# Kernel tuning notes

Hardware: AMD Instinct MI355X
Metric: run time of the kernel (lower is better)

Reference implementation:

```python
import jax, jax.numpy as jnp
import numpy as np

D_MODEL = 1024
N_HEADS = 16
HEAD_DIM = D_MODEL // N_HEADS


def setup_inputs() -> dict:
    key = jax.random.key(0)
    k1, k2, k3 = jax.random.split(key, 3)
    x = jax.random.normal(k1, (2, 2048, D_MODEL), dtype=jnp.float32)
    w_qkv = jax.random.normal(k2, (3 * D_MODEL, D_MODEL), dtype=jnp.float32) * 0.02
    w_out = jax.random.normal(k3, (D_MODEL, D_MODEL), dtype=jnp.float32) * 0.02
    return {"x": x, "w_qkv": w_qkv, "w_out": w_out}


def reference(x, w_qkv, w_out):
    B, T, D = x.shape
    H, Hd = N_HEADS, HEAD_DIM
    # QKV projection: Linear stores weight as [out, in] -> '...i,oi->...o'
    qkv = jnp.einsum('bti,oi->bto', x, w_qkv)              # [B, T, 3D]
    # split (3*H, Hs) group-major, chunk into q/k/v of H heads each
    qkv = qkv.reshape(B, T, 3, H, Hd)
    q = jnp.transpose(qkv[:, :, 0], (0, 2, 1, 3))          # [B, H, T, Hd]
    k = jnp.transpose(qkv[:, :, 1], (0, 2, 1, 3))
    v = jnp.transpose(qkv[:, :, 2], (0, 2, 1, 3))
    scale = 1.0 / jnp.sqrt(jnp.asarray(Hd, dtype=x.dtype))
    scores = jnp.einsum('bhqd,bhkd->bhqk', q, k) * scale   # [B, H, T, T]
    causal = jnp.tril(jnp.ones((T, T), dtype=bool))        # [T, T]
    scores = jnp.where(causal[None, None], scores, jnp.asarray(-jnp.inf, dtype=scores.dtype))
    attn = jax.nn.softmax(scores, axis=-1)
    ctx = jnp.einsum('bhqk,bhkd->bhqd', attn, v)           # [B, H, T, Hd]
    ctx = jnp.transpose(ctx, (0, 2, 1, 3)).reshape(B, T, D)
    return jnp.einsum('bti,oi->bto', ctx, w_out)
```

## Files before the change

kernel.cpp:

```cpp
#include <hip/hip_runtime.h>


typedef short short8 __attribute__((ext_vector_type(8)));
typedef float f32x4 __attribute__((ext_vector_type(4)));
typedef unsigned short u16;
typedef unsigned int u32;

#define T_SEQ 2048
#define N_B 2
#define N_H 16
#define HD 64
#define DM 1024
#define TRIPLE 3072

__device__ __forceinline__ u16 f2bf(float f) {
  union { float f; unsigned u; } v;
  v.f = f;
  unsigned r = v.u + 0x7fffu + ((v.u >> 16) & 1u);
  return (u16)(r >> 16);
}

__device__ __forceinline__ float bf2f(u16 x) {
  return __uint_as_float((u32)x << 16);
}

__device__ __forceinline__ u32 cvtpk(float a, float b) {
  u32 r;
  asm("v_cvt_pk_bf16_f32 %0, %1, %2" : "=v"(r) : "v"(a), "v"(b));
  return r;
}

typedef const __attribute__((address_space(1))) void gvoid;
typedef __attribute__((address_space(3))) void lvoid;

__device__ __forceinline__ void g2l16(const void* g, void* l) {
  __builtin_amdgcn_global_load_lds((gvoid*)g, (lvoid*)l, 16, 0, 0);
}

__device__ __forceinline__ void storeC(float* p, float v) { *p = v; }
__device__ __forceinline__ void storeC(u16* p, float v) { *p = f2bf(v); }

__global__ __launch_bounds__(256) void cast_all(const float4* __restrict__ x,
                                                const float4* __restrict__ wq,
                                                const float4* __restrict__ wo,
                                                ushort4* __restrict__ out) {
  int i = blockIdx.x * 256 + threadIdx.x;
  const float4* src;
  int off;
  if (i < 1048576) { src = x; off = 0; }
  else if (i < 1835008) { src = wq; off = 1048576; }
  else { src = wo; off = 1835008; }
  float4 v = src[i - off];
  ushort4 o;
  o.x = f2bf(v.x); o.y = f2bf(v.y); o.z = f2bf(v.z); o.w = f2bf(v.w);
  out[i] = o;
}

__global__ __launch_bounds__(256) void vtrans(const u16* __restrict__ qkv,
                                              u16* __restrict__ vT) {
  const int tid = threadIdx.x;
  const int w = tid >> 6, lane = tid & 63;
  const int ti = lane >> 3, di = lane & 7;
  const int h = blockIdx.y, b = blockIdx.z;
  const int t0 = blockIdx.x * 256 + w * 64 + ti * 8;

  const u16* src = qkv + (size_t)(b * T_SEQ + t0) * TRIPLE + 2 * DM + h * HD + di * 8;
  u32 x[8][4];
#pragma unroll
  for (int e = 0; e < 8; ++e) {
    union { short8 v; u32 u[4]; } cv;
    cv.v = *(const short8*)(src + (size_t)e * TRIPLE);
#pragma unroll
    for (int j = 0; j < 4; ++j) x[e][j] = cv.u[j];
  }
  u32 y[8][4];
#pragma unroll
  for (int a = 0; a < 4; ++a)
#pragma unroll
    for (int j = 0; j < 4; ++j) {
      u32 lo = x[2 * a][j], hi = x[2 * a + 1][j];
      y[2 * a][j] = (lo & 0x0000FFFFu) | (hi << 16);
      y[2 * a + 1][j] = (lo >> 16) | (hi & 0xFFFF0000u);
    }
  u16* dst = vT + ((size_t)(b * N_H + h) * HD + di * 8) * T_SEQ + t0;
#pragma unroll
  for (int dd = 0; dd < 8; ++dd) {
    union { short8 v; u32 u[4]; } cv;
#pragma unroll
    for (int a = 0; a < 4; ++a) cv.u[a] = y[2 * a + (dd & 1)][dd >> 1];
    *(short8*)(dst + (size_t)dd * T_SEQ) = cv.v;
  }
}

template <typename OutT>
__global__ __launch_bounds__(256) void gemm_bt(const u16* __restrict__ A,
                                               const u16* __restrict__ W,
                                               OutT* __restrict__ C,
                                               int M, int N, int K) {
  __shared__ char As[128 * 64 * 2];
  __shared__ char Bs[128 * 64 * 2];
  const int tid = threadIdx.x;
  const int lane = tid & 63, w = tid >> 6;
  const int l15 = lane & 15, l4 = lane >> 4;
  const int m0 = blockIdx.y * 128, n0 = blockIdx.x * 128;
  const int wr = (w >> 1) * 64, wc = (w & 1) * 64;

  const f32x4 zero = {0.f, 0.f, 0.f, 0.f};
  f32x4 acc[4][4];
#pragma unroll
  for (int m = 0; m < 4; ++m)
#pragma unroll
    for (int n = 0; n < 4; ++n) acc[m][n] = zero;

  for (int k0 = 0; k0 < K; k0 += 64) {
#pragma unroll
    for (int i = 0; i < 4; ++i) {
      const int cb = (i * 4 + w) * 64;
      const int c = cb + lane;
      const int row = c >> 3;
      const int ks = ((c & 7) ^ (row & 7)) * 8;
      g2l16(A + (size_t)(m0 + row) * K + k0 + ks, As + (size_t)cb * 16);
      g2l16(W + (size_t)(n0 + row) * K + k0 + ks, Bs + (size_t)cb * 16);
    }
    __syncthreads();

#pragma unroll
    for (int kk = 0; kk < 2; ++kk) {
      short8 a[4], b[4];
#pragma unroll
      for (int m = 0; m < 4; ++m) {
        int row = wr + m * 16 + l15;
        int slot = (kk * 4 + l4) ^ (row & 7);
        a[m] = *(const short8*)(As + row * 128 + slot * 16);
      }
#pragma unroll
      for (int n = 0; n < 4; ++n) {
        int row = wc + n * 16 + l15;
        int slot = (kk * 4 + l4) ^ (row & 7);
        b[n] = *(const short8*)(Bs + row * 128 + slot * 16);
      }
#pragma unroll
      for (int m = 0; m < 4; ++m)
#pragma unroll
        for (int n = 0; n < 4; ++n)
          acc[m][n] = __builtin_amdgcn_mfma_f32_16x16x32_bf16(a[m], b[n], acc[m][n], 0, 0, 0);
    }
    __syncthreads();
  }

#pragma unroll
  for (int m = 0; m < 4; ++m)
#pragma unroll
    for (int n = 0; n < 4; ++n)
#pragma unroll
      for (int r = 0; r < 4; ++r) {
        int row = m0 + wr + m * 16 + l4 * 4 + r;
        int col = n0 + wc + n * 16 + l15;
        storeC(C + (size_t)row * N + col, acc[m][n][r]);
      }
}

__global__ __launch_bounds__(128) void attn_fwd(const u16* __restrict__ qkv,
                                                const u16* __restrict__ vT,
                                                u16* __restrict__ ctx) {
  __shared__ char Ks[2][8192];
  __shared__ char Vs[2][8192];
  __shared__ char Pl[2][2048];

  const int tid = threadIdx.x;
  const int lane = tid & 63, w = tid >> 6;
  const int l15 = lane & 15, l4 = lane >> 4;
  const int g = blockIdx.x;
  const int p = blockIdx.y;
  const int h = g & 15, b = g >> 4;
  const int q0A = 32 * p, q0B = 32 * (63 - p);
  const int dA = p >> 1;

  const float c_log2 = 0.18033688011112042f;
  short8 qa2[2][2];
#pragma unroll
  for (int ps = 0; ps < 2; ++ps) {
    const int qq0 = ps ? q0B : q0A;
    const u16* qp = qkv + (size_t)(b * T_SEQ + qq0 + w * 16 + l15) * TRIPLE + h * HD;
#pragma unroll
    for (int kk = 0; kk < 2; ++kk) {
      short8 raw = *(const short8*)(qp + kk * 32 + l4 * 8);
      union { short8 v; u32 w4[4]; } qq;
#pragma unroll
      for (int j = 0; j < 4; ++j)
        qq.w4[j] = cvtpk(bf2f((u16)raw[2 * j]) * c_log2,
                         bf2f((u16)raw[2 * j + 1]) * c_log2);
      qa2[ps][kk] = qq.v;
    }
  }

  const int r0 = tid >> 3, c0 = tid & 7;
  const int swz = (c0 ^ (r0 & 7)) << 3;
  const u16* kbase = qkv + (size_t)(b * T_SEQ + r0) * TRIPLE + DM + h * HD + swz;
  const u16* vbase = vT + ((size_t)g * HD + r0) * T_SEQ + swz;

#define STAGE(kt_, buf_)                                                        \
  {                                                                             \
    _Pragma("unroll") for (int i_ = 0; i_ < 4; ++i_) {                          \
      g2l16(kbase + (size_t)((kt_) * 64 + 16 * i_) * TRIPLE,                    \
            Ks[buf_] + tid * 16 + i_ * 2048);                                   \
      g2l16(vbase + (size_t)(16 * i_) * T_SEQ + (kt_) * 64,                     \
            Vs[buf_] + tid * 16 + i_ * 2048);                                   \
    }                                                                           \
  }

  char* Plb = Pl[w];

  const f32x4 zero = {0.f, 0.f, 0.f, 0.f};
  f32x4 o[4];
#pragma unroll
  for (int nt = 0; nt < 4; ++nt) o[nt] = zero;
  float mr = -INFINITY, lr = 0.f;
  short8 qa0 = qa2[0][0], qa1 = qa2[0][1];
  int q0 = q0A;

  STAGE(0, 0);
  __syncthreads();
  int cur = 0;

  for (int i = 0;; ++i) {
    const int kt = (i <= dA) ? i : 32 - i;

    if (i < 32) {
      const int nkt = (i + 1 <= dA) ? i + 1 : 31 - i;
      STAGE(nkt, cur ^ 1);
    }

    f32x4 s[4];
#pragma unroll
    for (int mt = 0; mt < 4; ++mt) s[mt] = zero;
    __builtin_amdgcn_s_setprio(1);
#pragma unroll
    for (int mt = 0; mt < 4; ++mt) {
      int row = mt * 16 + l15;
      int slot0 = l4 ^ (row & 7);
      short8 kb0 = *(const short8*)(Ks[cur] + row * 128 + slot0 * 16);
      s[mt] = __builtin_amdgcn_mfma_f32_16x16x32_bf16(kb0, qa0, s[mt], 0, 0, 0);
      int slot1 = (4 + l4) ^ (row & 7);
      short8 kb1 = *(const short8*)(Ks[cur] + row * 128 + slot1 * 16);
      s[mt] = __builtin_amdgcn_mfma_f32_16x16x32_bf16(kb1, qa1, s[mt], 0, 0, 0);
    }
    __builtin_amdgcn_s_setprio(0);

    if (i == dA || i == dA + 1) {
      const int qrow = q0 + w * 16 + l15;
#pragma unroll
      for (int mt = 0; mt < 4; ++mt)
#pragma unroll
        for (int r = 0; r < 4; ++r) {
          int key = kt * 64 + mt * 16 + l4 * 4 + r;
          if (key > qrow) s[mt][r] = -INFINITY;
        }
    }

    float mx = fmaxf(fmaxf(fmaxf(s[0][0], s[0][1]), fmaxf(s[0][2], s[0][3])),
                     fmaxf(fmaxf(s[1][0], s[1][1]), fmaxf(s[1][2], s[1][3])));
    mx = fmaxf(mx, fmaxf(fmaxf(fmaxf(s[2][0], s[2][1]), fmaxf(s[2][2], s[2][3])),
                         fmaxf(fmaxf(s[3][0], s[3][1]), fmaxf(s[3][2], s[3][3]))));
    mx = fmaxf(mx, __shfl_xor(mx, 16));
    mx = fmaxf(mx, __shfl_xor(mx, 32));
    if (!__all(mx - mr <= 8.0f)) {
      float mn = fmaxf(mr, mx);
      float fr = exp2f(mr - mn);
      lr *= fr;
#pragma unroll
      for (int r = 0; r < 4; ++r) {
        float frq = __shfl(fr, l4 * 4 + r);
#pragma unroll
        for (int nt = 0; nt < 4; ++nt) o[nt][r] *= frq;
      }
      mr = mn;
    }
    float ps = 0.f;
#pragma unroll
    for (int mt = 0; mt < 4; ++mt)
#pragma unroll
      for (int r = 0; r < 4; ++r) {
        float pv = exp2f(s[mt][r] - mr);
        s[mt][r] = pv;
        ps += pv;
      }
    lr += ps;

#pragma unroll
    for (int mt = 0; mt < 4; ++mt) {
      uint2 pw;
      pw.x = cvtpk(s[mt][0], s[mt][1]);
      pw.y = cvtpk(s[mt][2], s[mt][3]);
      int slot = ((mt * 2 + (l4 >> 1)) ^ (l15 & 7));
      *(uint2*)(Plb + l15 * 128 + (slot << 4) + ((l4 & 1) << 3)) = pw;
    }

    __builtin_amdgcn_s_setprio(1);
#pragma unroll
    for (int kk = 0; kk < 2; ++kk) {
      short8 pa = *(const short8*)(Plb + l15 * 128 + (((kk * 4 + l4) ^ (l15 & 7)) << 4));
#pragma unroll
      for (int nt = 0; nt < 4; ++nt) {
        int d = nt * 16 + l15;
        int slot = (kk * 4 + l4) ^ (l15 & 7);
        short8 vb = *(const short8*)(Vs[cur] + d * 128 + slot * 16);
        o[nt] = __builtin_amdgcn_mfma_f32_16x16x32_bf16(pa, vb, o[nt], 0, 0, 0);
      }
    }
    __builtin_amdgcn_s_setprio(0);

    if (i == dA || i == 32) {
      lr += __shfl_xor(lr, 16);
      lr += __shfl_xor(lr, 32);
#pragma unroll
      for (int r = 0; r < 4; ++r) {
        float lrq = __shfl(lr, l4 * 4 + r);
        float inv = __builtin_amdgcn_rcpf(lrq);
        size_t t = (size_t)(b * T_SEQ + q0 + w * 16 + l4 * 4 + r);
#pragma unroll
        for (int nt = 0; nt < 4; ++nt)
          ctx[t * DM + h * HD + nt * 16 + l15] = f2bf(o[nt][r] * inv);
      }
      if (i == 32) break;
#pragma unroll
      for (int nt = 0; nt < 4; ++nt) o[nt] = zero;
      mr = -INFINITY; lr = 0.f;
      qa0 = qa2[1][0]; qa1 = qa2[1][1];
      q0 = q0B;
    }

    __syncthreads();
    cur ^= 1;
  }
#undef STAGE
}

extern "C" void kernel_launch(void* const* d_in, const int* in_sizes, int n_in,
                              void* d_out, int out_size, void* d_ws, size_t ws_size,
                              hipStream_t stream) {
  const float* x = (const float*)d_in[0];
  const float* wqkv = (const float*)d_in[1];
  const float* wout = (const float*)d_in[2];
  float* out = (float*)d_out;
  char* ws = (char*)d_ws;

  u16* xb    = (u16*)(ws);
  u16* wqkvb = (u16*)(ws + 8u * 1024 * 1024);
  u16* woutb = (u16*)(ws + 14u * 1024 * 1024);
  u16* qkvb  = (u16*)(ws + 16u * 1024 * 1024);
  u16* ctxb  = (u16*)(ws + 40u * 1024 * 1024);
  u16* vTb   = (u16*)(ws + 48u * 1024 * 1024);

  cast_all<<<8192, 256, 0, stream>>>((const float4*)x, (const float4*)wqkv,
                                     (const float4*)wout, (ushort4*)xb);

  gemm_bt<u16><<<dim3(24, 32), 256, 0, stream>>>(xb, wqkvb, qkvb, 4096, 3072, 1024);

  vtrans<<<dim3(8, N_H, N_B), 256, 0, stream>>>(qkvb, vTb);

  attn_fwd<<<dim3(32, 32), 128, 0, stream>>>(qkvb, vTb, ctxb);

  gemm_bt<float><<<dim3(8, 32), 256, 0, stream>>>(ctxb, woutb, out, 4096, 1024, 1024);
}
```

Measured before the change: 132.4 us.

## Use 32x32 MFMA with register-resident P and triple-buffered K/V in attention

Attention now uses 32x32x16 bf16 MFMAs, with each wave covering 32 query rows and each block covering 64-row query tiles (paired causal tiles). The P matrix is passed to the PV MFMA through permlane32 swaps instead of a round trip through shared memory. The row max and sum now need only one cross-lane shuffle. K/V staging moves from double to triple buffering, with vmcnt-based waits that keep two tiles in flight. The grid is halved, so fewer blocks give less parallelism, and each wave carries more registers in exchange for fewer LDS accesses and instructions.

```diff
diff --git a/kernel.cpp b/kernel.cpp
--- a/kernel.cpp
+++ b/kernel.cpp
@@ -3,6 +3,8 @@
 
 typedef short short8 __attribute__((ext_vector_type(8)));
 typedef float f32x4 __attribute__((ext_vector_type(4)));
+typedef float f32x16 __attribute__((ext_vector_type(16)));
+typedef unsigned int u32x2 __attribute__((ext_vector_type(2)));
 typedef unsigned short u16;
 typedef unsigned int u32;
 
@@ -28,6 +30,12 @@
   u32 r;
   asm("v_cvt_pk_bf16_f32 %0, %1, %2" : "=v"(r) : "v"(a), "v"(b));
   return r;
+}
+
+__device__ __forceinline__ void pl32swap(u32& a, u32& b) {
+  u32x2 r = __builtin_amdgcn_permlane32_swap(a, b, false, false);
+  a = r[0];
+  b = r[1];
 }
 
 typedef const __attribute__((address_space(1))) void gvoid;
@@ -163,34 +171,32 @@
 __global__ __launch_bounds__(128) void attn_fwd(const u16* __restrict__ qkv,
                                                 const u16* __restrict__ vT,
                                                 u16* __restrict__ ctx) {
-  __shared__ char Ks[2][8192];
-  __shared__ char Vs[2][8192];
-  __shared__ char Pl[2][2048];
+  __shared__ char Ks[3][8192];
+  __shared__ char Vs[3][8192];
 
   const int tid = threadIdx.x;
   const int lane = tid & 63, w = tid >> 6;
-  const int l15 = lane & 15, l4 = lane >> 4;
+  const int l31 = lane & 31, hi = lane >> 5;
   const int g = blockIdx.x;
   const int p = blockIdx.y;
   const int h = g & 15, b = g >> 4;
-  const int q0A = 32 * p, q0B = 32 * (63 - p);
-  const int dA = p >> 1;
+  const int q0A = 64 * p, q0B = 64 * (31 - p);
 
   const float c_log2 = 0.18033688011112042f;
-  short8 qa2[2][2];
+  short8 qa2[2][4];
 #pragma unroll
   for (int ps = 0; ps < 2; ++ps) {
     const int qq0 = ps ? q0B : q0A;
-    const u16* qp = qkv + (size_t)(b * T_SEQ + qq0 + w * 16 + l15) * TRIPLE + h * HD;
-#pragma unroll
-    for (int kk = 0; kk < 2; ++kk) {
-      short8 raw = *(const short8*)(qp + kk * 32 + l4 * 8);
+    const u16* qp = qkv + (size_t)(b * T_SEQ + qq0 + w * 32 + l31) * TRIPLE + h * HD + hi * 8;
+#pragma unroll
+    for (int kst = 0; kst < 4; ++kst) {
+      short8 raw = *(const short8*)(qp + kst * 16);
       union { short8 v; u32 w4[4]; } qq;
 #pragma unroll
       for (int j = 0; j < 4; ++j)
         qq.w4[j] = cvtpk(bf2f((u16)raw[2 * j]) * c_log2,
                          bf2f((u16)raw[2 * j + 1]) * c_log2);
-      qa2[ps][kk] = qq.v;
+      qa2[ps][kst] = qq.v;
     }
   }
 
@@ -203,135 +209,147 @@
   {                                                                             \
     _Pragma("unroll") for (int i_ = 0; i_ < 4; ++i_) {                          \
       g2l16(kbase + (size_t)((kt_) * 64 + 16 * i_) * TRIPLE,                    \
-            Ks[buf_] + tid * 16 + i_ * 2048);                                   \
+            Ks[buf_] + tid * 16 + 2048 * i_);                                   \
       g2l16(vbase + (size_t)(16 * i_) * T_SEQ + (kt_) * 64,                     \
-            Vs[buf_] + tid * 16 + i_ * 2048);                                   \
+            Vs[buf_] + tid * 16 + 2048 * i_);                                   \
     }                                                                           \
   }
 
-  char* Plb = Pl[w];
-
-  const f32x4 zero = {0.f, 0.f, 0.f, 0.f};
-  f32x4 o[4];
-#pragma unroll
-  for (int nt = 0; nt < 4; ++nt) o[nt] = zero;
+  const f32x16 zero16 = {0,0,0,0,0,0,0,0,0,0,0,0,0,0,0,0};
+  f32x16 o[2];
+  o[0] = zero16; o[1] = zero16;
   float mr = -INFINITY, lr = 0.f;
-  short8 qa0 = qa2[0][0], qa1 = qa2[0][1];
+  short8 qa_0 = qa2[0][0], qa_1 = qa2[0][1], qa_2 = qa2[0][2], qa_3 = qa2[0][3];
   int q0 = q0A;
 
   STAGE(0, 0);
-  __syncthreads();
+  {
+    const int kt1 = (1 <= p) ? 1 : 31;
+    STAGE(kt1, 1);
+  }
+  asm volatile("s_waitcnt vmcnt(8)\n\ts_barrier" ::: "memory");
+
   int cur = 0;
-
   for (int i = 0;; ++i) {
-    const int kt = (i <= dA) ? i : 32 - i;
-
-    if (i < 32) {
-      const int nkt = (i + 1 <= dA) ? i + 1 : 31 - i;
-      STAGE(nkt, cur ^ 1);
-    }
-
-    f32x4 s[4];
-#pragma unroll
-    for (int mt = 0; mt < 4; ++mt) s[mt] = zero;
+    const int kt = (i <= p) ? i : 32 - i;
+
+    if (i + 2 <= 32) {
+      const int nkt2 = (i + 2 <= p) ? i + 2 : 30 - i;
+      int sb = cur - 1;
+      if (sb < 0) sb = 2;
+      STAGE(nkt2, sb);
+    }
+
+    f32x16 s[2];
+    s[0] = zero16; s[1] = zero16;
     __builtin_amdgcn_s_setprio(1);
 #pragma unroll
-    for (int mt = 0; mt < 4; ++mt) {
-      int row = mt * 16 + l15;
-      int slot0 = l4 ^ (row & 7);
-      short8 kb0 = *(const short8*)(Ks[cur] + row * 128 + slot0 * 16);
-      s[mt] = __builtin_amdgcn_mfma_f32_16x16x32_bf16(kb0, qa0, s[mt], 0, 0, 0);
-      int slot1 = (4 + l4) ^ (row & 7);
-      short8 kb1 = *(const short8*)(Ks[cur] + row * 128 + slot1 * 16);
-      s[mt] = __builtin_amdgcn_mfma_f32_16x16x32_bf16(kb1, qa1, s[mt], 0, 0, 0);
+    for (int kst = 0; kst < 4; ++kst) {
+      const short8 qa = (kst == 0) ? qa_0 : (kst == 1) ? qa_1 : (kst == 2) ? qa_2 : qa_3;
+      const int slot = ((kst * 2 + hi) ^ (l31 & 7)) << 4;
+      short8 k0f = *(const short8*)(Ks[cur] + l31 * 128 + slot);
+      s[0] = __builtin_amdgcn_mfma_f32_32x32x16_bf16(k0f, qa, s[0], 0, 0, 0);
+      short8 k1f = *(const short8*)(Ks[cur] + (32 + l31) * 128 + slot);
+      s[1] = __builtin_amdgcn_mfma_f32_32x32x16_bf16(k1f, qa, s[1], 0, 0, 0);
     }
     __builtin_amdgcn_s_setprio(0);
 
-    if (i == dA || i == dA + 1) {
-      const int qrow = q0 + w * 16 + l15;
-#pragma unroll
-      for (int mt = 0; mt < 4; ++mt)
-#pragma unroll
-        for (int r = 0; r < 4; ++r) {
-          int key = kt * 64 + mt * 16 + l4 * 4 + r;
-          if (key > qrow) s[mt][r] = -INFINITY;
-        }
-    }
-
-    float mx = fmaxf(fmaxf(fmaxf(s[0][0], s[0][1]), fmaxf(s[0][2], s[0][3])),
-                     fmaxf(fmaxf(s[1][0], s[1][1]), fmaxf(s[1][2], s[1][3])));
-    mx = fmaxf(mx, fmaxf(fmaxf(fmaxf(s[2][0], s[2][1]), fmaxf(s[2][2], s[2][3])),
-                         fmaxf(fmaxf(s[3][0], s[3][1]), fmaxf(s[3][2], s[3][3]))));
-    mx = fmaxf(mx, __shfl_xor(mx, 16));
+    if (i == p || i == p + 1) {
+      const int qrow = q0 + w * 32 + l31;
+      const int kb0 = kt * 64 + 4 * hi;
+#pragma unroll
+      for (int r = 0; r < 16; ++r) {
+        const int key = kb0 + (r & 3) + 8 * (r >> 2);
+        if (key > qrow) s[0][r] = -INFINITY;
+        if (key + 32 > qrow) s[1][r] = -INFINITY;
+      }
+    }
+
+    float tA = fmaxf(s[0][0], s[1][0]);
+    float tB = fmaxf(s[0][1], s[1][1]);
+    float tC = fmaxf(s[0][2], s[1][2]);
+    float tD = fmaxf(s[0][3], s[1][3]);
+#pragma unroll
+    for (int r = 4; r < 16; r += 4) {
+      tA = fmaxf(tA, fmaxf(s[0][r], s[1][r]));
+      tB = fmaxf(tB, fmaxf(s[0][r + 1], s[1][r + 1]));
+      tC = fmaxf(tC, fmaxf(s[0][r + 2], s[1][r + 2]));
+      tD = fmaxf(tD, fmaxf(s[0][r + 3], s[1][r + 3]));
+    }
+    float mx = fmaxf(fmaxf(tA, tB), fmaxf(tC, tD));
     mx = fmaxf(mx, __shfl_xor(mx, 32));
     if (!__all(mx - mr <= 8.0f)) {
-      float mn = fmaxf(mr, mx);
-      float fr = exp2f(mr - mn);
+      const float mn = fmaxf(mr, mx);
+      const float fr = exp2f(mr - mn);
       lr *= fr;
 #pragma unroll
-      for (int r = 0; r < 4; ++r) {
-        float frq = __shfl(fr, l4 * 4 + r);
-#pragma unroll
-        for (int nt = 0; nt < 4; ++nt) o[nt][r] *= frq;
-      }
+      for (int r = 0; r < 16; ++r) { o[0][r] *= fr; o[1][r] *= fr; }
       mr = mn;
     }
-    float ps = 0.f;
-#pragma unroll
-    for (int mt = 0; mt < 4; ++mt)
-#pragma unroll
-      for (int r = 0; r < 4; ++r) {
-        float pv = exp2f(s[mt][r] - mr);
-        s[mt][r] = pv;
-        ps += pv;
-      }
-    lr += ps;
-
-#pragma unroll
-    for (int mt = 0; mt < 4; ++mt) {
-      uint2 pw;
-      pw.x = cvtpk(s[mt][0], s[mt][1]);
-      pw.y = cvtpk(s[mt][2], s[mt][3]);
-      int slot = ((mt * 2 + (l4 >> 1)) ^ (l15 & 7));
-      *(uint2*)(Plb + l15 * 128 + (slot << 4) + ((l4 & 1) << 3)) = pw;
+    {
+      float pA = 0.f, pB = 0.f, pC = 0.f, pD = 0.f;
+#pragma unroll
+      for (int r = 0; r < 16; r += 4) {
+        s[0][r] = exp2f(s[0][r] - mr); pA += s[0][r];
+        s[0][r + 1] = exp2f(s[0][r + 1] - mr); pB += s[0][r + 1];
+        s[0][r + 2] = exp2f(s[0][r + 2] - mr); pC += s[0][r + 2];
+        s[0][r + 3] = exp2f(s[0][r + 3] - mr); pD += s[0][r + 3];
+        s[1][r] = exp2f(s[1][r] - mr); pA += s[1][r];
+        s[1][r + 1] = exp2f(s[1][r + 1] - mr); pB += s[1][r + 1];
+        s[1][r + 2] = exp2f(s[1][r + 2] - mr); pC += s[1][r + 2];
+        s[1][r + 3] = exp2f(s[1][r + 3] - mr); pD += s[1][r + 3];
+      }
+      lr += (pA + pB) + (pC + pD);
     }
 
     __builtin_amdgcn_s_setprio(1);
 #pragma unroll
-    for (int kk = 0; kk < 2; ++kk) {
-      short8 pa = *(const short8*)(Plb + l15 * 128 + (((kk * 4 + l4) ^ (l15 & 7)) << 4));
-#pragma unroll
-      for (int nt = 0; nt < 4; ++nt) {
-        int d = nt * 16 + l15;
-        int slot = (kk * 4 + l4) ^ (l15 & 7);
-        short8 vb = *(const short8*)(Vs[cur] + d * 128 + slot * 16);
-        o[nt] = __builtin_amdgcn_mfma_f32_16x16x32_bf16(pa, vb, o[nt], 0, 0, 0);
+    for (int kf = 0; kf < 2; ++kf) {
+#pragma unroll
+      for (int sub = 0; sub < 2; ++sub) {
+        const int base = 8 * sub;
+        u32 w00 = cvtpk(s[kf][base + 0], s[kf][base + 1]);
+        u32 w01 = cvtpk(s[kf][base + 2], s[kf][base + 3]);
+        u32 w10 = cvtpk(s[kf][base + 4], s[kf][base + 5]);
+        u32 w11 = cvtpk(s[kf][base + 6], s[kf][base + 7]);
+        pl32swap(w00, w10);
+        pl32swap(w01, w11);
+        union { u32 u[4]; short8 v; } pw;
+        pw.u[0] = w00; pw.u[1] = w01; pw.u[2] = w10; pw.u[3] = w11;
+        const int ks = kf * 2 + sub;
+        const int vslot = (((ks * 2 + hi) ^ (l31 & 7)) << 4);
+        short8 v0 = *(const short8*)(Vs[cur] + l31 * 128 + vslot);
+        o[0] = __builtin_amdgcn_mfma_f32_32x32x16_bf16(v0, pw.v, o[0], 0, 0, 0);
+        short8 v1 = *(const short8*)(Vs[cur] + (32 + l31) * 128 + vslot);
+        o[1] = __builtin_amdgcn_mfma_f32_32x32x16_bf16(v1, pw.v, o[1], 0, 0, 0);
       }
     }
     __builtin_amdgcn_s_setprio(0);
 
-    if (i == dA || i == 32) {
-      lr += __shfl_xor(lr, 16);
-      lr += __shfl_xor(lr, 32);
-#pragma unroll
-      for (int r = 0; r < 4; ++r) {
-        float lrq = __shfl(lr, l4 * 4 + r);
-        float inv = __builtin_amdgcn_rcpf(lrq);
-        size_t t = (size_t)(b * T_SEQ + q0 + w * 16 + l4 * 4 + r);
-#pragma unroll
-        for (int nt = 0; nt < 4; ++nt)
-          ctx[t * DM + h * HD + nt * 16 + l15] = f2bf(o[nt][r] * inv);
-      }
+    if (i == p || i == 32) {
+      const float lf = lr + __shfl_xor(lr, 32);
+      const float inv = __builtin_amdgcn_rcpf(lf);
+      u16* crow = ctx + (size_t)(b * T_SEQ + q0 + w * 32 + l31) * DM + h * HD;
+#pragma unroll
+      for (int df = 0; df < 2; ++df)
+#pragma unroll
+        for (int r = 0; r < 16; r += 2) {
+          const int d = df * 32 + (r & 3) + 8 * (r >> 2) + 4 * hi;
+          u32 pk = cvtpk(o[df][r] * inv, o[df][r + 1] * inv);
+          *(u32*)(crow + d) = pk;
+        }
       if (i == 32) break;
-#pragma unroll
-      for (int nt = 0; nt < 4; ++nt) o[nt] = zero;
+      o[0] = zero16; o[1] = zero16;
       mr = -INFINITY; lr = 0.f;
-      qa0 = qa2[1][0]; qa1 = qa2[1][1];
+      qa_0 = qa2[1][0]; qa_1 = qa2[1][1]; qa_2 = qa2[1][2]; qa_3 = qa2[1][3];
       q0 = q0B;
     }
 
-    __syncthreads();
-    cur ^= 1;
+    if (i == 31)
+      asm volatile("s_waitcnt vmcnt(0)\n\ts_barrier" ::: "memory");
+    else
+      asm volatile("s_waitcnt vmcnt(8)\n\ts_barrier" ::: "memory");
+    cur = (cur == 2) ? 0 : cur + 1;
   }
 #undef STAGE
 }
@@ -359,7 +377,7 @@
 
   vtrans<<<dim3(8, N_H, N_B), 256, 0, stream>>>(qkvb, vTb);
 
-  attn_fwd<<<dim3(32, 32), 128, 0, stream>>>(qkvb, vTb, ctxb);
+  attn_fwd<<<dim3(32, 16), 128, 0, stream>>>(qkvb, vTb, ctxb);
 
   gemm_bt<float><<<dim3(8, 32), 256, 0, stream>>>(ctxb, woutb, out, 4096, 1024, 1024);
 }
```

Result: slower. 146.8 us (+10.8%).
